# Kernel tuning notes

Measured on AMD Instinct MI355X. Metric: run time of the kernel, lower is better.

## Reference

```python
import jax, jax.numpy as jnp
import numpy as np

N = 2048       # num nodes
IN = 512       # in_features == hidden_features == out_features (residuals)
HID = 512
OUT = 512
H = 8          # num_heads
DX = 256       # x feature dim
LN_EPS = 1e-5
NORM_EPS = 1e-12


def _layernorm(x, g, b):
    mu = jnp.mean(x, axis=-1, keepdims=True)
    var = jnp.mean(jnp.square(x - mu), axis=-1, keepdims=True)
    return (x - mu) * jax.lax.rsqrt(var + LN_EPS) * g + b


def _l1_normalize(x):
    # torch F.normalize(p=1): x / max(||x||_1, eps)
    n = jnp.sum(jnp.abs(x), axis=-1, keepdims=True)
    return x / jnp.maximum(n, NORM_EPS)


def _linear_init(key, out_f, in_f):
    kw, kb = jax.random.split(key)
    bound = 1.0 / np.sqrt(in_f)
    W = jax.random.uniform(kw, (out_f, in_f), jnp.float32, -bound, bound)
    b = jax.random.uniform(kb, (out_f,), jnp.float32, -bound, bound)
    return W, b


def setup_inputs() -> dict:
    key = jax.random.key(0)
    ks = jax.random.split(key, 10)
    h = jax.random.normal(ks[0], (N, IN), jnp.float32)
    x = jax.random.uniform(ks[1], (N, DX), jnp.float32)
    Wk, bk = _linear_init(ks[2], HID, IN)
    Wq, bq = _linear_init(ks[3], HID, IN)
    Wv, bv = _linear_init(ks[4], HID, IN)
    Wm1, bm1 = _linear_init(ks[5], H, H + 1)   # mixing_x2h
    Wm2, bm2 = _linear_init(ks[6], 1, H)
    Wfc, bfc = _linear_init(ks[7], OUT, HID + 4)
    ln_g = jnp.ones((IN,), jnp.float32)
    ln_b = jnp.zeros((IN,), jnp.float32)
    lnf_g = jnp.ones((HID,), jnp.float32)
    lnf_b = jnp.zeros((HID,), jnp.float32)
    return dict(h=h, x=x, ln_g=ln_g, ln_b=ln_b, Wk=Wk, bk=bk, Wq=Wq, bq=bq,
                Wv=Wv, bv=bv, Wm1=Wm1, bm1=bm1, Wm2=Wm2, bm2=bm2,
                lnf_g=lnf_g, lnf_b=lnf_b, Wfc=Wfc, bfc=bfc)


def reference(h, x, ln_g, ln_b, Wk, bk, Wq, bq, Wv, bv, Wm1, bm1, Wm2, bm2,
              lnf_g, lnf_b, Wfc, bfc):
    h0, x0 = h, x
    hn = _layernorm(h, ln_g, ln_b)
    xn = _l1_normalize(x)

    k = (hn @ Wk.T + bk).reshape(N, HID // H, H)
    q = (hn @ Wq.T + bq).reshape(N, HID // H, H)
    a_h = jnp.einsum('xyb,zyb->xzb', k, q)          # [N, N, H]
    a_x = xn @ xn.T                                  # [N, N]

    # head mixing: Linear(H+1 -> H) over concat([a_x, a_h])
    a_cat = jnp.concatenate([a_x[..., None], a_h], axis=-1)  # [N, N, H+1]
    a_h = a_cat @ Wm1.T + bm1                                # [N, N, H]
    a_x = (a_h @ Wm2.T + bm2)[..., 0] + a_x                  # [N, N]

    a_h = jax.nn.softmax(a_h, axis=-1)               # softmax over heads
    a_x = _l1_normalize(a_x)

    # per-row stats of a_x -> [N, 4]
    i = jnp.concatenate([
        jnp.diagonal(a_x)[:, None],
        jnp.sum(a_x, axis=-1, keepdims=True),
        jnp.std(a_x, axis=-1, ddof=1, keepdims=True),
        jnp.max(a_x, axis=-1, keepdims=True),
    ], axis=-1)

    v = (hn @ Wv.T + bv).reshape(N, OUT // H, H)
    hm = jnp.einsum('xyb,yzb->xzb', a_h, v).reshape(N, HID)
    xm = a_x @ xn

    hm = hm + h0
    xm = xm + x0
    _h0 = hm

    hf = _layernorm(hm, lnf_g, lnf_b)
    hf = jnp.concatenate([hf, i], axis=-1)           # [N, HID+4]
    hf = jax.nn.elu(hf @ Wfc.T + bfc)
    hf = hf + _h0
    return (hf, xm)
```

## Files before the change

### kernel.cpp

```cpp
#include <hip/hip_runtime.h>
#include <math.h>

#define NN 2048
#define FD 512
#define DXF 256
#define JC 8
#define CHKJ (NN/JC)
#define ITI 32
#define JTW 64
#define NIT (CHKJ/JTW)
#define KC (NN/4)

typedef unsigned short u16;
typedef unsigned int u32;
typedef __attribute__((ext_vector_type(8))) short s16x8;
typedef __attribute__((ext_vector_type(4))) float f32x4;

__device__ __forceinline__ f32x4 MFMA16(s16x8 a, s16x8 b, f32x4 c) {
  return __builtin_amdgcn_mfma_f32_16x16x32_bf16(a, b, c, 0, 0, 0);
}
__device__ __forceinline__ float blo(u32 u) { return __uint_as_float(u << 16); }
__device__ __forceinline__ float bhi(u32 u) { return __uint_as_float(u & 0xffff0000u); }
__device__ __forceinline__ float b2f(u16 v) { return __uint_as_float((u32)v << 16); }
__device__ __forceinline__ u16 bf1(float f) {
  u32 u = __float_as_uint(f);
  u += 0x7fffu + ((u >> 16) & 1u);
  return (u16)(u >> 16);
}
__device__ __forceinline__ u32 pkbf(float a, float b) {
  u32 ua = __float_as_uint(a), ub = __float_as_uint(b);
  ua += 0x7fffu + ((ua >> 16) & 1u);
  ub += 0x7fffu + ((ub >> 16) & 1u);
  return (ua >> 16) | (ub & 0xffff0000u);
}

__global__ void preproc_k(
    const float* __restrict__ h, const float* __restrict__ ln_g,
    const float* __restrict__ ln_b, u16* __restrict__ hnB,
    const float* __restrict__ x, u16* __restrict__ xnB,
    const float* __restrict__ Wk, const float* __restrict__ Wq,
    const float* __restrict__ Wv, u16* __restrict__ wkB, u16* __restrict__ wqB,
    u16* __restrict__ wvB, const float* __restrict__ Wfc, u16* __restrict__ wfcB) {
  int bid = blockIdx.x, t = threadIdx.x;
  __shared__ float red[4][2];
  if (bid < NN) {
    int r = bid;
    float2 v = ((const float2*)(h + (size_t)r * FD))[t];
    float2 w = make_float2(v.x + v.y, v.x * v.x + v.y * v.y);
#pragma unroll
    for (int o = 32; o > 0; o >>= 1) { w.x += __shfl_xor(w.x, o); w.y += __shfl_xor(w.y, o); }
    if ((t & 63) == 0) { red[t >> 6][0] = w.x; red[t >> 6][1] = w.y; }
    __syncthreads();
    float S  = (red[0][0] + red[1][0]) + (red[2][0] + red[3][0]);
    float SQ = (red[0][1] + red[1][1]) + (red[2][1] + red[3][1]);
    float mean = S * (1.f / FD);
    float var  = SQ * (1.f / FD) - mean * mean;
    float rs = rsqrtf(var + 1e-5f);
    float2 gg = ((const float2*)ln_g)[t], bb = ((const float2*)ln_b)[t];
    float ox = (v.x - mean) * rs * gg.x + bb.x;
    float oy = (v.y - mean) * rs * gg.y + bb.y;
    *(u32*)(hnB + (size_t)r * FD + 2 * t) = pkbf(ox, oy);
  } else if (bid < 2 * NN) {
    int r = bid - NN;
    float v = x[(size_t)r * DXF + t];
    float s = fabsf(v);
#pragma unroll
    for (int o = 32; o > 0; o >>= 1) s += __shfl_xor(s, o);
    if ((t & 63) == 0) red[t >> 6][0] = s;
    __syncthreads();
    float S = (red[0][0] + red[1][0]) + (red[2][0] + red[3][0]);
    float inv = 1.f / fmaxf(S, 1e-12f);
    xnB[(size_t)r * DXF + t] = bf1(v * inv);
  } else if (bid < 2 * NN + 1536) {
    int idx = bid - 2 * NN;
    int z = idx >> 9;
    int i = ((idx & 511) << 8) + t;
    const float* W = (z == 0) ? Wk : (z == 1) ? Wq : Wv;
    u16* O = (z == 0) ? wkB : (z == 1) ? wqB : wvB;
    float2 v = ((const float2*)W)[i];
    ((u32*)O)[i] = pkbf(v.x, v.y);
  } else {
    int i = (bid - (2 * NN + 1536)) * 256 + t;
    if (i < 512 * 272) {
      int r = i / 272, c2 = (i - r * 272) * 2;
      float a = (c2 < 516) ? Wfc[r * 516 + c2] : 0.f;
      float b = (c2 + 1 < 516) ? Wfc[r * 516 + c2 + 1] : 0.f;
      ((u32*)wfcB)[i] = pkbf(a, b);
    }
  }
}

__global__ void xnt_k(const u16* __restrict__ xnB, u16* __restrict__ xnTg,
                      u16* __restrict__ xnF) {
  __shared__ u16 tile[16][264];
  int t = threadIdx.x;
  int r0 = blockIdx.x * 16;
#pragma unroll
  for (int s = 0; s < 2; ++s) {
    int c = s * 256 + t;
    int db = c & 31, row = c >> 5;
    *(uint4*)&tile[row][db * 8] = *(const uint4*)(xnB + (size_t)(r0 + row) * DXF + db * 8);
  }
  __syncthreads();
#pragma unroll
  for (int s = 0; s < 2; ++s) {
    int c = s * 256 + t;
    int jb = c & 1, d = c >> 1;
    u32 p[4];
#pragma unroll
    for (int e2 = 0; e2 < 4; ++e2) {
      u16 a = tile[jb * 8 + e2 * 2][d], b = tile[jb * 8 + e2 * 2 + 1][d];
      p[e2] = (u32)a | ((u32)b << 16);
    }
    *(uint4*)(xnTg + (size_t)d * NN + r0 + jb * 8) = make_uint4(p[0], p[1], p[2], p[3]);
  }
#pragma unroll
  for (int s = 0; s < 2; ++s) {
    int idx = s * 256 + t;
    int ks = idx >> 6, lane = idx & 63;
    int row = lane & 15, db = ks * 32 + (lane >> 4) * 8;
    uint4 v = *(const uint4*)&tile[row][db];
    *(uint4*)(xnF + (((size_t)(r0 >> 4) * 8 + ks) * 64 + lane) * 8) = v;
  }
}

__global__ __launch_bounds__(256) void proj3_k(
    const u16* __restrict__ A,
    const u16* __restrict__ W0, const u16* __restrict__ W1, const u16* __restrict__ W2,
    const float* __restrict__ b0, const float* __restrict__ b1, const float* __restrict__ b2,
    u16* __restrict__ kP, u16* __restrict__ qF, u16* __restrict__ vF) {
  int z = blockIdx.z;
  const u16* B = (z == 0) ? W0 : (z == 1) ? W1 : W2;
  const float* bias = (z == 0) ? b0 : (z == 1) ? b1 : b2;
  int t = threadIdx.x, w = t >> 6, lane = t & 63, g = lane >> 4, li = lane & 15;
  int m0 = blockIdx.x * 64 + (w & 1) * 32;
  int n0 = blockIdx.y * 64 + (w >> 1) * 32;
  f32x4 acc[2][2] = {};
  for (int k0 = 0; k0 < FD; k0 += 32) {
    s16x8 a0 = *(const s16x8*)(A + (size_t)(m0 + li) * FD + k0 + g * 8);
    s16x8 a1 = *(const s16x8*)(A + (size_t)(m0 + 16 + li) * FD + k0 + g * 8);
    s16x8 bA = *(const s16x8*)(B + (size_t)(n0 + li) * FD + k0 + g * 8);
    s16x8 bB = *(const s16x8*)(B + (size_t)(n0 + 16 + li) * FD + k0 + g * 8);
    acc[0][0] = MFMA16(a0, bA, acc[0][0]);
    acc[0][1] = MFMA16(a0, bB, acc[0][1]);
    acc[1][0] = MFMA16(a1, bA, acc[1][0]);
    acc[1][1] = MFMA16(a1, bB, acc[1][1]);
  }
#pragma unroll
  for (int ms = 0; ms < 2; ++ms)
#pragma unroll
    for (int ns = 0; ns < 2; ++ns) {
      int ncol = n0 + ns * 16 + li;
      float bv = bias[ncol];
      if (z == 0) {
#pragma unroll
        for (int r = 0; r < 4; ++r) {
          int i = m0 + ms * 16 + g * 4 + r;
          kP[((size_t)(ncol & 7) * NN + i) * 64 + (ncol >> 3)] = bf1(acc[ms][ns][r] + bv);
        }
      } else if (z == 1) {
#pragma unroll
        for (int r = 0; r < 4; ++r) {
          int i = m0 + ms * 16 + g * 4 + r;
          size_t idx = ((size_t)(i >> 4) * 8 + (ncol & 7)) * 1024 +
                       (size_t)(ncol >> 8) * 512 +
                       (size_t)((i & 15) | (((ncol >> 6) & 3) << 4)) * 8 +
                       ((ncol >> 3) & 7);
          qF[idx] = bf1(acc[ms][ns][r] + bv);
        }
      } else {
        u16 e4[4];
#pragma unroll
        for (int r = 0; r < 4; ++r) e4[r] = bf1(acc[ms][ns][r] + bv);
        u32 p0 = (u32)e4[0] | ((u32)e4[1] << 16);
        u32 p1 = (u32)e4[2] | ((u32)e4[3] << 16);
        int ibase = m0 + ms * 16 + g * 4;
        int lane_w = ((ncol >> 3) & 15) | (((ibase >> 3) & 3) << 4);
        size_t base = ((((size_t)(m0 >> 5) * 8 + (ncol & 7)) * 4 + (ncol >> 7)) * 64 + lane_w) * 8 +
                      ((g & 1) * 4);
        *(uint2*)(vF + base) = make_uint2(p0, p1);
      }
    }
}

__global__ __launch_bounds__(256) void fc_gemm_k(
    const u16* __restrict__ A, const u16* __restrict__ B,
    const float* __restrict__ bias, const float* __restrict__ res,
    float* __restrict__ C) {
  int t = threadIdx.x, w = t >> 6, lane = t & 63, g = lane >> 4, li = lane & 15;
  int m0 = blockIdx.x * 32 + (w & 1) * 16;
  int n0 = blockIdx.y * 32 + (w >> 1) * 16;
  f32x4 acc = {};
  for (int k0 = 0; k0 < 544; k0 += 32) {
    s16x8 a0 = *(const s16x8*)(A + (size_t)(m0 + li) * 544 + k0 + g * 8);
    s16x8 b0 = *(const s16x8*)(B + (size_t)(n0 + li) * 544 + k0 + g * 8);
    acc = MFMA16(a0, b0, acc);
  }
  int ncol = n0 + li;
  float bv = bias[ncol];
#pragma unroll
  for (int r = 0; r < 4; ++r) {
    int i = m0 + g * 4 + r;
    float cv = acc[r] + bv;
    cv = (cv > 0.f) ? cv : (expf(cv) - 1.f);
    cv += res[(size_t)i * FD + ncol];
    C[(size_t)i * FD + ncol] = cv;
  }
}

__global__ __launch_bounds__(256) void xm_split_k(
    const u16* __restrict__ axg, const u16* __restrict__ xnTg,
    float* __restrict__ xmp, float* __restrict__ stq) {
  int t = threadIdx.x, w = t >> 6, lane = t & 63, g = lane >> 4, li = lane & 15;
  int m0 = blockIdx.x * 64 + (w & 1) * 32;
  int n0 = blockIdx.y * 64 + (w >> 1) * 32;
  int z = blockIdx.z;
  const int kb = z * KC;
  f32x4 acc[2][2] = {};
  float sab[2] = {0.f, 0.f}, ssu[2] = {0.f, 0.f}, ssq[2] = {0.f, 0.f};
  float smx[2] = {-1e30f, -1e30f};
  const bool do_stats = (blockIdx.y == 0) && ((w >> 1) == 0);
  for (int k0 = 0; k0 < KC; k0 += 32) {
    s16x8 a0 = *(const s16x8*)(axg + (size_t)(m0 + li) * NN + kb + k0 + g * 8);
    s16x8 a1 = *(const s16x8*)(axg + (size_t)(m0 + 16 + li) * NN + kb + k0 + g * 8);
    s16x8 bA = *(const s16x8*)(xnTg + (size_t)(n0 + li) * NN + kb + k0 + g * 8);
    s16x8 bB = *(const s16x8*)(xnTg + (size_t)(n0 + 16 + li) * NN + kb + k0 + g * 8);
    acc[0][0] = MFMA16(a0, bA, acc[0][0]);
    acc[0][1] = MFMA16(a0, bB, acc[0][1]);
    acc[1][0] = MFMA16(a1, bA, acc[1][0]);
    acc[1][1] = MFMA16(a1, bB, acc[1][1]);
    if (do_stats) {
#pragma unroll
      for (int ms = 0; ms < 2; ++ms) {
        u32 pu[4];
        *(s16x8*)pu = ms ? a1 : a0;
#pragma unroll
        for (int q2 = 0; q2 < 4; ++q2) {
          float x0 = blo(pu[q2]), x1 = bhi(pu[q2]);
          sab[ms] += fabsf(x0) + fabsf(x1);
          ssu[ms] += x0 + x1;
          ssq[ms] += x0 * x0 + x1 * x1;
          smx[ms] = fmaxf(smx[ms], fmaxf(x0, x1));
        }
      }
    }
  }
  if (do_stats) {
#pragma unroll
    for (int off = 16; off < 64; off <<= 1) {
#pragma unroll
      for (int ms = 0; ms < 2; ++ms) {
        sab[ms] += __shfl_xor(sab[ms], off);
        ssu[ms] += __shfl_xor(ssu[ms], off);
        ssq[ms] += __shfl_xor(ssq[ms], off);
        smx[ms] = fmaxf(smx[ms], __shfl_xor(smx[ms], off));
      }
    }
    if (g == 0) {
#pragma unroll
      for (int ms = 0; ms < 2; ++ms) {
        size_t base = ((size_t)z * NN + m0 + ms * 16 + li) * 4;
        stq[base + 0] = sab[ms]; stq[base + 1] = ssu[ms];
        stq[base + 2] = ssq[ms]; stq[base + 3] = smx[ms];
      }
    }
  }
#pragma unroll
  for (int ms = 0; ms < 2; ++ms)
#pragma unroll
    for (int ns = 0; ns < 2; ++ns) {
      int ncol = n0 + ns * 16 + li;
#pragma unroll
      for (int r = 0; r < 4; ++r) {
        int i = m0 + ms * 16 + g * 4 + r;
        xmp[(size_t)z * NN * DXF + (size_t)i * DXF + ncol] = acc[ms][ns][r];
      }
    }
}

__global__ __launch_bounds__(512, 2) void fused_mfma_k(
    const u16* __restrict__ kP, const u16* __restrict__ qF,
    const u16* __restrict__ vF, const u16* __restrict__ xnB,
    const u16* __restrict__ xnF,
    const float* __restrict__ Wm1, const float* __restrict__ bm1,
    const float* __restrict__ Wm2, const float* __restrict__ bm2,
    u16* __restrict__ hmPart, u16* __restrict__ axg, float* __restrict__ stPd) {
  __shared__ __align__(16) unsigned char L[81920];
  const int O_KI = 0, O_XNI = 32768, O_P = 49152;
  const int t = threadIdx.x, w = t >> 6, lane = t & 63;
  const int g = lane >> 4, li = lane & 15;
  const int i0 = blockIdx.x * ITI, chunk = blockIdx.y;
  const int si = w & 1;
  const int jw = w >> 1;
  const int jL = jw * 16 + li;
  const int iRow = si * 16 + li;
  const int prow = si * 16 + li;

  float W1[8][9], B1v[8], w2v[8];
#pragma unroll
  for (int o = 0; o < 8; ++o) {
    B1v[o] = bm1[o];
    w2v[o] = Wm2[o];
#pragma unroll
    for (int b3 = 0; b3 < 9; ++b3) W1[o][b3] = Wm1[o * 9 + b3];
  }
  const float b2v = bm2[0];

#pragma unroll
  for (int s = 0; s < 4; ++s) {
    int c = s * 512 + t;
    int yb = c & 7, il = (c >> 3) & 31, b = c >> 8;
    uint4 v = *(const uint4*)(kP + ((size_t)b * NN + i0 + il) * 64 + yb * 8);
    *(uint4*)(L + O_KI + b * 4096 + il * 128 + ((yb ^ (il & 7)) << 4)) = v;
  }
#pragma unroll
  for (int s = 0; s < 2; ++s) {
    int c = s * 512 + t;
    int db = c & 31, il = c >> 5;
    uint4 v = *(const uint4*)(xnB + (size_t)(i0 + il) * DXF + db * 8);
    *(uint4*)(L + O_XNI + il * 512 + ((db ^ (il & 7)) << 4)) = v;
  }
  __syncthreads();

  f32x4 hmA[2][4];
#pragma unroll
  for (int a = 0; a < 2; ++a)
#pragma unroll
    for (int c = 0; c < 4; ++c) hmA[a][c] = (f32x4)(0.f);

  for (int it = 0; it < NIT; ++it) {
    const int j0 = chunk * CHKJ + it * JTW;
    const int jt = (j0 >> 4) + jw;
    const int jb32 = j0 >> 5;
    f32x4 accS[9];
#pragma unroll
    for (int a = 0; a < 9; ++a) accS[a] = (f32x4)(0.f);
#pragma unroll
    for (int b = 0; b < 8; ++b)
#pragma unroll
      for (int ks = 0; ks < 2; ++ks) {
        int blk = ks * 4 + g;
        s16x8 af = *(const s16x8*)(L + O_KI + b * 4096 + iRow * 128 +
                                   ((blk ^ (iRow & 7)) << 4));
        s16x8 bf = *(const s16x8*)(qF + (((size_t)jt * 8 + b) * 2 + ks) * 512 +
                                   (size_t)lane * 8);
        accS[b] = MFMA16(af, bf, accS[b]);
      }
#pragma unroll
    for (int ks = 0; ks < 8; ++ks) {
      int blk = ks * 4 + g;
      s16x8 af = *(const s16x8*)(L + O_XNI + iRow * 512 + ((blk ^ (iRow & 7)) << 4));
      s16x8 bf = *(const s16x8*)(xnF + ((size_t)jt * 8 + ks) * 512 + (size_t)lane * 8);
      accS[8] = MFMA16(af, bf, accS[8]);
    }
    s16x8 vf0[2][4];
#pragma unroll
    for (int kb = 0; kb < 2; ++kb)
#pragma unroll
      for (int zt = 0; zt < 4; ++zt)
        vf0[kb][zt] = *(const s16x8*)(vF + ((((size_t)(jb32 + kb) * 8 + jw * 2 + 0) * 4 + zt) * 512) +
                                      (size_t)lane * 8);
    __syncthreads();
#pragma unroll
    for (int r = 0; r < 4; ++r) {
      float sb[8];
#pragma unroll
      for (int b = 0; b < 8; ++b) sb[b] = accS[b][r];
      float ax = accS[8][r];
      float m[8];
#pragma unroll
      for (int o = 0; o < 8; ++o) {
        float a = B1v[o] + W1[o][0] * ax;
#pragma unroll
        for (int b = 0; b < 8; ++b) a += W1[o][1 + b] * sb[b];
        m[o] = a;
      }
      float axn = b2v + ax;
#pragma unroll
      for (int o = 0; o < 8; ++o) axn += w2v[o] * m[o];
      const int iL2 = si * 16 + g * 4 + r;
      const int iG = i0 + iL2, jG = j0 + jL;
      axg[(size_t)iG * NN + jG] = bf1(axn);
      if (iG == jG) stPd[iG] = axn;
      float mx = m[0];
#pragma unroll
      for (int o = 1; o < 8; ++o) mx = fmaxf(mx, m[o]);
      float es[8], esum = 0.f;
#pragma unroll
      for (int o = 0; o < 8; ++o) { es[o] = __expf(m[o] - mx); esum += es[o]; }
      float inv = 1.f / esum;
      const int base = iL2 * 128 + (((jL >> 3) ^ (iL2 & 7)) << 4) + (jL & 7) * 2;
#pragma unroll
      for (int b = 0; b < 8; ++b)
        *(u16*)(L + O_P + b * 4096 + base) = bf1(es[b] * inv);
    }
    s16x8 vf1[2][4];
#pragma unroll
    for (int kb = 0; kb < 2; ++kb)
#pragma unroll
      for (int zt = 0; zt < 4; ++zt)
        vf1[kb][zt] = *(const s16x8*)(vF + ((((size_t)(jb32 + kb) * 8 + jw * 2 + 1) * 4 + zt) * 512) +
                                      (size_t)lane * 8);
    __syncthreads();
#pragma unroll
    for (int hh = 0; hh < 2; ++hh) {
      const int hd = jw * 2 + hh;
#pragma unroll
      for (int kb = 0; kb < 2; ++kb) {
        s16x8 pa = *(const s16x8*)(L + O_P + hd * 4096 + prow * 128 +
                                   (((kb * 4 + g) ^ (prow & 7)) << 4));
#pragma unroll
        for (int zt = 0; zt < 4; ++zt) {
          s16x8 vf = hh ? vf1[kb][zt] : vf0[kb][zt];
          hmA[hh][zt] = MFMA16(pa, vf, hmA[hh][zt]);
        }
      }
    }
  }
#pragma unroll
  for (int hh = 0; hh < 2; ++hh) {
    const int hd = jw * 2 + hh;
#pragma unroll
    for (int zt = 0; zt < 4; ++zt)
#pragma unroll
      for (int r = 0; r < 4; ++r) {
        int i = i0 + si * 16 + g * 4 + r;
        int z = zt * 16 + li;
        hmPart[((size_t)(chunk * 8 + hd) * NN + i) * 64 + z] = bf1(hmA[hh][zt][r]);
      }
  }
}

__global__ void epilogue1_k(
    const float* __restrict__ h, const float* __restrict__ x,
    const u16* __restrict__ hmp, const float* __restrict__ xmp,
    const float* __restrict__ stq, const float* __restrict__ stPd,
    const float* __restrict__ lnf_g, const float* __restrict__ lnf_b,
    float* __restrict__ hmf, u16* __restrict__ hfeB, float* __restrict__ out_xm) {
  int r = blockIdx.x, t = threadIdx.x;
  int c0 = 2 * t, c1 = c0 + 1;
  float2 acc = ((const float2*)(h + (size_t)r * FD))[t];
#pragma unroll
  for (int ch = 0; ch < JC; ++ch) {
    acc.x += b2f(hmp[((size_t)(ch * 8 + (c0 & 7)) * NN + r) * 64 + (c0 >> 3)]);
    acc.y += b2f(hmp[((size_t)(ch * 8 + (c1 & 7)) * NN + r) * 64 + (c1 >> 3)]);
  }
  ((float2*)(hmf + (size_t)r * FD))[t] = acc;
  float2 w = make_float2(acc.x + acc.y, acc.x * acc.x + acc.y * acc.y);
#pragma unroll
  for (int o = 32; o > 0; o >>= 1) { w.x += __shfl_xor(w.x, o); w.y += __shfl_xor(w.y, o); }
  __shared__ float red[4][2];
  __shared__ float s_inv;
  if ((t & 63) == 0) { red[t >> 6][0] = w.x; red[t >> 6][1] = w.y; }
  __syncthreads();
  float S  = (red[0][0] + red[1][0]) + (red[2][0] + red[3][0]);
  float SQ = (red[0][1] + red[1][1]) + (red[2][1] + red[3][1]);
  float mean = S * (1.f / FD);
  float var  = SQ * (1.f / FD) - mean * mean;
  float rs = rsqrtf(var + 1e-5f);
  float2 g2 = ((const float2*)lnf_g)[t], b2 = ((const float2*)lnf_b)[t];
  float ox = (acc.x - mean) * rs * g2.x + b2.x;
  float oy = (acc.y - mean) * rs * g2.y + b2.y;
  *(u32*)(hfeB + (size_t)r * 544 + c0) = pkbf(ox, oy);
  if (t == 0) {
    float sab = 0.f, ssu = 0.f, ssq = 0.f, smx = -1e30f;
#pragma unroll
    for (int c = 0; c < 4; ++c) {
      size_t b = ((size_t)c * NN + r) * 4;
      sab += stq[b + 0]; ssu += stq[b + 1]; ssq += stq[b + 2];
      smx = fmaxf(smx, stq[b + 3]);
    }
    float diag = stPd[r];
    float L1 = fmaxf(sab, 1e-12f);
    float inv = 1.f / L1;
    float stdv = sqrtf(fmaxf((ssq - ssu * ssu * (1.f / 2048.f)) * (1.f / 2047.f), 0.f)) * inv;
    u16* he = hfeB + (size_t)r * 544;
    he[512] = bf1(diag * inv); he[513] = bf1(ssu * inv);
    he[514] = bf1(stdv);       he[515] = bf1(smx * inv);
    s_inv = inv;
  }
  if (t < 14) *(u32*)(hfeB + (size_t)r * 544 + 516 + 2 * t) = 0;
  __syncthreads();
  float inv = s_inv;
  float xv = xmp[(size_t)r * DXF + t] + xmp[(size_t)NN * DXF + (size_t)r * DXF + t] +
             xmp[2 * (size_t)NN * DXF + (size_t)r * DXF + t] +
             xmp[3 * (size_t)NN * DXF + (size_t)r * DXF + t];
  out_xm[(size_t)r * DXF + t] = xv * inv + x[(size_t)r * DXF + t];
}

extern "C" void kernel_launch(void* const* d_in, const int* in_sizes, int n_in,
                              void* d_out, int out_size, void* d_ws, size_t ws_size,
                              hipStream_t stream) {
  (void)in_sizes; (void)n_in; (void)out_size; (void)ws_size;
  const float* h    = (const float*)d_in[0];
  const float* x    = (const float*)d_in[1];
  const float* ln_g = (const float*)d_in[2];
  const float* ln_b = (const float*)d_in[3];
  const float* Wk   = (const float*)d_in[4];
  const float* bk   = (const float*)d_in[5];
  const float* Wq   = (const float*)d_in[6];
  const float* bq   = (const float*)d_in[7];
  const float* Wv   = (const float*)d_in[8];
  const float* bv   = (const float*)d_in[9];
  const float* Wm1  = (const float*)d_in[10];
  const float* bm1  = (const float*)d_in[11];
  const float* Wm2  = (const float*)d_in[12];
  const float* bm2  = (const float*)d_in[13];
  const float* lnf_g = (const float*)d_in[14];
  const float* lnf_b = (const float*)d_in[15];
  const float* Wfc  = (const float*)d_in[16];
  const float* bfc  = (const float*)d_in[17];

  char* wsb = (char*)d_ws;
  size_t off = 0;
  auto alloc = [&](size_t bytes) { char* p = wsb + off; off += (bytes + 255) & ~(size_t)255; return p; };
  u16*   hnB  = (u16*)alloc((size_t)NN * FD * 2);
  u16*   wkB  = (u16*)alloc((size_t)FD * FD * 2);
  u16*   wqB  = (u16*)alloc((size_t)FD * FD * 2);
  u16*   wvB  = (u16*)alloc((size_t)FD * FD * 2);
  u16*   wfcB = (u16*)alloc((size_t)512 * 544 * 2);
  u16*   kP   = (u16*)alloc((size_t)8 * NN * 64 * 2);
  u16*   qF   = (u16*)alloc((size_t)8 * NN * 64 * 2);
  u16*   vF   = (u16*)alloc((size_t)8 * 64 * NN * 2);
  u16*   xnB  = (u16*)alloc((size_t)NN * DXF * 2);
  u16*   xnTg = (u16*)alloc((size_t)DXF * NN * 2);
  u16*   xnF  = (u16*)alloc((size_t)NN * DXF * 2);
  u16*   axg  = (u16*)alloc((size_t)NN * NN * 2);
  u16*   hmp  = (u16*)alloc((size_t)JC * 8 * NN * 64 * 2);
  float* xmp  = (float*)alloc((size_t)4 * NN * DXF * 4);
  float* stq  = (float*)alloc((size_t)4 * NN * 4 * 4);
  float* stPd = (float*)alloc((size_t)NN * 4);
  float* hmf  = (float*)alloc((size_t)NN * FD * 4);
  u16*   hfeB = (u16*)alloc((size_t)NN * 544 * 2);
  float* out_hf = (float*)d_out;
  float* out_xm = out_hf + (size_t)NN * FD;

  preproc_k<<<2 * NN + 1536 + 544, 256, 0, stream>>>(
      h, ln_g, ln_b, hnB, x, xnB, Wk, Wq, Wv, wkB, wqB, wvB, Wfc, wfcB);
  xnt_k<<<NN / 16, 256, 0, stream>>>(xnB, xnTg, xnF);

  proj3_k<<<dim3(32, 8, 3), 256, 0, stream>>>(hnB, wkB, wqB, wvB, bk, bq, bv, kP, qF, vF);

  fused_mfma_k<<<dim3(NN / ITI, JC), 512, 0, stream>>>(kP, qF, vF, xnB, xnF,
                                                       Wm1, bm1, Wm2, bm2,
                                                       hmp, axg, stPd);

  xm_split_k<<<dim3(32, 4, 4), 256, 0, stream>>>(axg, xnTg, xmp, stq);

  epilogue1_k<<<NN, 256, 0, stream>>>(h, x, hmp, xmp, stq, stPd, lnf_g, lnf_b, hmf, hfeB, out_xm);

  fc_gemm_k<<<dim3(64, 16), 256, 0, stream>>>(hfeB, wfcB, bfc, hmf, out_hf);
}
```

Before: 141.7 us.

## Keep softmax probabilities in registers and feed PV MFMA directly via transposed score tiles

Swaps the MFMA operand roles so the score tile's output layout matches the A-operand layout of a 16x16x16 bf16 MFMA. The per-head probabilities can then be packed in registers and fed straight into the PV product, with no LDS staging. The two mid-loop barriers and 32KB of shared memory go away, and the vF layout is re-tiled to match. In exchange, each wave now accumulates all 8 heads (32 f32x4 accumulators, more register pressure). A cross-wave LDS reduction over the four j-subtiles is added at the end, before writing hmPart.

```diff
diff --git a/kernel.cpp b/kernel.cpp
--- a/kernel.cpp
+++ b/kernel.cpp
@@ -14,10 +14,14 @@
 typedef unsigned short u16;
 typedef unsigned int u32;
 typedef __attribute__((ext_vector_type(8))) short s16x8;
+typedef __attribute__((ext_vector_type(4))) short s16x4;
 typedef __attribute__((ext_vector_type(4))) float f32x4;
 
 __device__ __forceinline__ f32x4 MFMA16(s16x8 a, s16x8 b, f32x4 c) {
   return __builtin_amdgcn_mfma_f32_16x16x32_bf16(a, b, c, 0, 0, 0);
+}
+__device__ __forceinline__ f32x4 MFMA16K16(s16x4 a, s16x4 b, f32x4 c) {
+  return __builtin_amdgcn_mfma_f32_16x16x16bf16_1k(a, b, c, 0, 0, 0);
 }
 __device__ __forceinline__ float blo(u32 u) { return __uint_as_float(u << 16); }
 __device__ __forceinline__ float bhi(u32 u) { return __uint_as_float(u & 0xffff0000u); }
@@ -174,11 +178,9 @@
         for (int r = 0; r < 4; ++r) e4[r] = bf1(acc[ms][ns][r] + bv);
         u32 p0 = (u32)e4[0] | ((u32)e4[1] << 16);
         u32 p1 = (u32)e4[2] | ((u32)e4[3] << 16);
-        int ibase = m0 + ms * 16 + g * 4;
-        int lane_w = ((ncol >> 3) & 15) | (((ibase >> 3) & 3) << 4);
-        size_t base = ((((size_t)(m0 >> 5) * 8 + (ncol & 7)) * 4 + (ncol >> 7)) * 64 + lane_w) * 8 +
-                      ((g & 1) * 4);
-        *(uint2*)(vF + base) = make_uint2(p0, p1);
+        size_t idx = ((((size_t)((m0 >> 4) + ms) * 8 + (ncol & 7)) * 4 + ((ncol >> 7) & 3)) * 64 +
+                      (size_t)(((ncol >> 3) & 15) | (g << 4))) * 4;
+        *(uint2*)(vF + idx) = make_uint2(p0, p1);
       }
     }
 }
@@ -285,16 +287,15 @@
     const float* __restrict__ Wm1, const float* __restrict__ bm1,
     const float* __restrict__ Wm2, const float* __restrict__ bm2,
     u16* __restrict__ hmPart, u16* __restrict__ axg, float* __restrict__ stPd) {
-  __shared__ __align__(16) unsigned char L[81920];
-  const int O_KI = 0, O_XNI = 32768, O_P = 49152;
+  __shared__ __align__(16) unsigned char L[49152];
+  const int O_KI = 0, O_XNI = 32768;
+  float* LF = (float*)L;
   const int t = threadIdx.x, w = t >> 6, lane = t & 63;
   const int g = lane >> 4, li = lane & 15;
   const int i0 = blockIdx.x * ITI, chunk = blockIdx.y;
-  const int si = w & 1;
-  const int jw = w >> 1;
-  const int jL = jw * 16 + li;
+  const int si = w >> 2, jw = w & 3;
   const int iRow = si * 16 + li;
-  const int prow = si * 16 + li;
+  const int iG = i0 + iRow;
 
   float W1[8][9], B1v[8], w2v[8];
 #pragma unroll
@@ -322,16 +323,16 @@
   }
   __syncthreads();
 
-  f32x4 hmA[2][4];
-#pragma unroll
-  for (int a = 0; a < 2; ++a)
+  f32x4 hmA[8][4];
+#pragma unroll
+  for (int a = 0; a < 8; ++a)
 #pragma unroll
     for (int c = 0; c < 4; ++c) hmA[a][c] = (f32x4)(0.f);
 
   for (int it = 0; it < NIT; ++it) {
     const int j0 = chunk * CHKJ + it * JTW;
     const int jt = (j0 >> 4) + jw;
-    const int jb32 = j0 >> 5;
+    const int jbase = j0 + jw * 16;
     f32x4 accS[9];
 #pragma unroll
     for (int a = 0; a < 9; ++a) accS[a] = (f32x4)(0.f);
@@ -340,27 +341,20 @@
 #pragma unroll
       for (int ks = 0; ks < 2; ++ks) {
         int blk = ks * 4 + g;
-        s16x8 af = *(const s16x8*)(L + O_KI + b * 4096 + iRow * 128 +
+        s16x8 af = *(const s16x8*)(qF + (((size_t)jt * 8 + b) * 2 + ks) * 512 +
+                                   (size_t)lane * 8);
+        s16x8 bf = *(const s16x8*)(L + O_KI + b * 4096 + iRow * 128 +
                                    ((blk ^ (iRow & 7)) << 4));
-        s16x8 bf = *(const s16x8*)(qF + (((size_t)jt * 8 + b) * 2 + ks) * 512 +
-                                   (size_t)lane * 8);
         accS[b] = MFMA16(af, bf, accS[b]);
       }
 #pragma unroll
     for (int ks = 0; ks < 8; ++ks) {
       int blk = ks * 4 + g;
-      s16x8 af = *(const s16x8*)(L + O_XNI + iRow * 512 + ((blk ^ (iRow & 7)) << 4));
-      s16x8 bf = *(const s16x8*)(xnF + ((size_t)jt * 8 + ks) * 512 + (size_t)lane * 8);
+      s16x8 af = *(const s16x8*)(xnF + ((size_t)jt * 8 + ks) * 512 + (size_t)lane * 8);
+      s16x8 bf = *(const s16x8*)(L + O_XNI + iRow * 512 + ((blk ^ (iRow & 7)) << 4));
       accS[8] = MFMA16(af, bf, accS[8]);
     }
-    s16x8 vf0[2][4];
-#pragma unroll
-    for (int kb = 0; kb < 2; ++kb)
-#pragma unroll
-      for (int zt = 0; zt < 4; ++zt)
-        vf0[kb][zt] = *(const s16x8*)(vF + ((((size_t)(jb32 + kb) * 8 + jw * 2 + 0) * 4 + zt) * 512) +
-                                      (size_t)lane * 8);
-    __syncthreads();
+    u32 pb2[8][2], ax2[2];
 #pragma unroll
     for (int r = 0; r < 4; ++r) {
       float sb[8];
@@ -378,10 +372,10 @@
       float axn = b2v + ax;
 #pragma unroll
       for (int o = 0; o < 8; ++o) axn += w2v[o] * m[o];
-      const int iL2 = si * 16 + g * 4 + r;
-      const int iG = i0 + iL2, jG = j0 + jL;
-      axg[(size_t)iG * NN + jG] = bf1(axn);
+      const int jG = jbase + g * 4 + r;
       if (iG == jG) stPd[iG] = axn;
+      u16 axv = bf1(axn);
+      if (r & 1) ax2[r >> 1] |= (u32)axv << 16; else ax2[r >> 1] = axv;
       float mx = m[0];
 #pragma unroll
       for (int o = 1; o < 8; ++o) mx = fmaxf(mx, m[o]);
@@ -389,45 +383,44 @@
 #pragma unroll
       for (int o = 0; o < 8; ++o) { es[o] = __expf(m[o] - mx); esum += es[o]; }
       float inv = 1.f / esum;
-      const int base = iL2 * 128 + (((jL >> 3) ^ (iL2 & 7)) << 4) + (jL & 7) * 2;
-#pragma unroll
-      for (int b = 0; b < 8; ++b)
-        *(u16*)(L + O_P + b * 4096 + base) = bf1(es[b] * inv);
-    }
-    s16x8 vf1[2][4];
-#pragma unroll
-    for (int kb = 0; kb < 2; ++kb)
-#pragma unroll
-      for (int zt = 0; zt < 4; ++zt)
-        vf1[kb][zt] = *(const s16x8*)(vF + ((((size_t)(jb32 + kb) * 8 + jw * 2 + 1) * 4 + zt) * 512) +
-                                      (size_t)lane * 8);
+#pragma unroll
+      for (int o = 0; o < 8; ++o) {
+        u16 pv = bf1(es[o] * inv);
+        if (r & 1) pb2[o][r >> 1] |= (u32)pv << 16; else pb2[o][r >> 1] = pv;
+      }
+    }
+    *(uint2*)(axg + (size_t)iG * NN + jbase + g * 4) = make_uint2(ax2[0], ax2[1]);
+#pragma unroll
+    for (int hd = 0; hd < 8; ++hd) {
+      uint2 pu = make_uint2(pb2[hd][0], pb2[hd][1]);
+      s16x4 pa = *(s16x4*)&pu;
+#pragma unroll
+      for (int zt = 0; zt < 4; ++zt) {
+        s16x4 vb = *(const s16x4*)(vF + ((((size_t)jt * 8 + hd) * 4 + zt) * 64 +
+                                         (size_t)lane) * 4);
+        hmA[hd][zt] = MFMA16K16(pa, vb, hmA[hd][zt]);
+      }
+    }
+  }
+
+  for (int hd = 0; hd < 8; ++hd) {
     __syncthreads();
 #pragma unroll
-    for (int hh = 0; hh < 2; ++hh) {
-      const int hd = jw * 2 + hh;
-#pragma unroll
-      for (int kb = 0; kb < 2; ++kb) {
-        s16x8 pa = *(const s16x8*)(L + O_P + hd * 4096 + prow * 128 +
-                                   (((kb * 4 + g) ^ (prow & 7)) << 4));
-#pragma unroll
-        for (int zt = 0; zt < 4; ++zt) {
-          s16x8 vf = hh ? vf1[kb][zt] : vf0[kb][zt];
-          hmA[hh][zt] = MFMA16(pa, vf, hmA[hh][zt]);
-        }
-      }
-    }
-  }
-#pragma unroll
-  for (int hh = 0; hh < 2; ++hh) {
-    const int hd = jw * 2 + hh;
-#pragma unroll
     for (int zt = 0; zt < 4; ++zt)
 #pragma unroll
-      for (int r = 0; r < 4; ++r) {
-        int i = i0 + si * 16 + g * 4 + r;
-        int z = zt * 16 + li;
-        hmPart[((size_t)(chunk * 8 + hd) * NN + i) * 64 + z] = bf1(hmA[hh][zt][r]);
-      }
+      for (int r = 0; r < 4; ++r)
+        LF[(w * 16 + g * 4 + r) * 64 + zt * 16 + li] = hmA[hd][zt][r];
+    __syncthreads();
+#pragma unroll
+    for (int u = 0; u < 4; ++u) {
+      int flat = u * 512 + t;
+      int si2 = flat >> 10, rest = flat & 1023, ii = rest >> 6, zz = rest & 63;
+      float s = LF[((si2 * 4 + 0) * 16 + ii) * 64 + zz] +
+                LF[((si2 * 4 + 1) * 16 + ii) * 64 + zz] +
+                LF[((si2 * 4 + 2) * 16 + ii) * 64 + zz] +
+                LF[((si2 * 4 + 3) * 16 + ii) * 64 + zz];
+      hmPart[((size_t)(chunk * 8 + hd) * NN + i0 + si2 * 16 + ii) * 64 + zz] = bf1(s);
+    }
   }
 }
 
```

Result: slower. 224.5 us (+58.5%).
